# Performance work log

Measured on AMD Instinct MI355X. Metric: run time of the kernel, lower is better.

## Reference

```python
import jax, jax.numpy as jnp
import numpy as np

N = 100000   # num_nodes
E = 1250000  # num_edges
D = 64       # embedding_dim
L = 3        # num_layers


def setup_inputs() -> dict:
    key = jax.random.key(0)
    k1, k2, k3, k4 = jax.random.split(key, 4)
    edge_index = jax.random.randint(k1, (2, E), 0, N, dtype=jnp.int64)
    edge_label_index = jax.random.randint(k2, (2, E), 0, N, dtype=jnp.int64)
    # xavier_uniform init of Embedding(N, D)
    bound = float(np.sqrt(6.0 / (N + D)))
    emb_weight = jax.random.uniform(k3, (N, D), jnp.float32, -bound, bound)
    alpha = jnp.full((L + 1,), 1.0 / (L + 1), dtype=jnp.float32)
    return {"edge_index": edge_index, "edge_label_index": edge_label_index,
            "emb_weight": emb_weight, "alpha": alpha}


def reference(edge_index, edge_label_index, emb_weight, alpha):
    src, dst = edge_index[0], edge_index[1]
    n = emb_weight.shape[0]
    # gcn_norm (LGConv, no self-loops): deg over destination, sym normalization
    deg = jax.ops.segment_sum(jnp.ones(src.shape[0], emb_weight.dtype), dst, num_segments=n)
    dis = jnp.where(deg > 0, jax.lax.rsqrt(jnp.where(deg > 0, deg, 1.0)), 0.0)
    w = dis[src] * dis[dst]  # [E]

    weights = jax.nn.softmax(alpha)  # [L+1]
    x = emb_weight
    out = x * weights[0]
    for i in range(L):
        # LGConv: out[dst] += norm * x[src]
        x = jax.ops.segment_sum(w[:, None] * x[src], dst, num_segments=n)
        out = out + x * weights[i + 1]

    # predict_link_embedding: per-edge dot product
    return (out[edge_label_index[0]] * out[edge_label_index[1]]).sum(axis=-1)
```

## Files before the change

kernel.cpp:

```cpp
#include <hip/hip_runtime.h>
#include <math.h>

#define DIM 64
#define PART_T 2048
#define BK_SHIFT 9
#define BK_SPAN 512
#define BK_CAP 8192
#define BK_PAD 2048
#define BK_REG (BK_CAP + BK_PAD)
#define CSR_T 1024

typedef _Float16 half8 __attribute__((ext_vector_type(8)));


__device__ __forceinline__ half8 shfl_xor_h8(half8 v, int mask) {
    int4 iv;
    __builtin_memcpy(&iv, &v, 16);
    iv.x = __shfl_xor(iv.x, mask, 64);
    iv.y = __shfl_xor(iv.y, mask, 64);
    iv.z = __shfl_xor(iv.z, mask, 64);
    iv.w = __shfl_xor(iv.w, mask, 64);
    half8 r;
    __builtin_memcpy(&r, &iv, 16);
    return r;
}

__device__ __forceinline__ half8 dpp_ror8_h8(half8 v) {
    int4 iv;
    __builtin_memcpy(&iv, &v, 16);
    int4 r;
    r.x = __builtin_amdgcn_update_dpp(0, iv.x, 0x128, 0xF, 0xF, true);
    r.y = __builtin_amdgcn_update_dpp(0, iv.y, 0x128, 0xF, 0xF, true);
    r.z = __builtin_amdgcn_update_dpp(0, iv.z, 0x128, 0xF, 0xF, true);
    r.w = __builtin_amdgcn_update_dpp(0, iv.w, 0x128, 0xF, 0xF, true);
    half8 out;
    __builtin_memcpy(&out, &r, 16);
    return out;
}

__device__ __forceinline__ float dpp_sum8_f32(float v) {
    int x = __float_as_int(v);
    v += __int_as_float(__builtin_amdgcn_update_dpp(0, x, 0xB1, 0xF, 0xF, true));
    x = __float_as_int(v);
    v += __int_as_float(__builtin_amdgcn_update_dpp(0, x, 0x4E, 0xF, 0xF, true));
    x = __float_as_int(v);
    v += __int_as_float(__builtin_amdgcn_update_dpp(0, x, 0x141, 0xF, 0xF, true));
    return v;
}

__device__ __forceinline__ int wave_incl_scan(int v) {
    int lane = threadIdx.x & 63;
    #pragma unroll
    for (int d = 1; d < 64; d <<= 1) {
        int n = __shfl_up(v, d, 64);
        if (lane >= d) v += n;
    }
    return v;
}

__device__ __forceinline__ int block_scan_excl(int v, int* wsum) {
    int incl = wave_incl_scan(v);
    int w = threadIdx.x >> 6;
    if ((threadIdx.x & 63) == 63) wsum[w] = incl;
    __syncthreads();
    int offset = 0;
    #pragma unroll
    for (int i = 0; i < 3; ++i) offset += (i < w) ? wsum[i] : 0;
    return offset + incl - v;
}

template <int NW>
__device__ __forceinline__ int block_scan_excl_n(int v, int* wsum) {
    int incl = wave_incl_scan(v);
    int w = threadIdx.x >> 6;
    if ((threadIdx.x & 63) == 63) wsum[w] = incl;
    __syncthreads();
    int offset = 0;
    #pragma unroll
    for (int i = 0; i < NW - 1; ++i) offset += (i < w) ? wsum[i] : 0;
    return offset + incl - v;
}


__global__ void init_kernel(int* __restrict__ gcursor, int K,
                            half8* __restrict__ g0, half8* __restrict__ g1,
                            half8* __restrict__ g2, int N) {
    int t = threadIdx.x;
    if (t < K) gcursor[t] = t * BK_CAP;
    if (t < 8) {
        half8 z = (half8)(_Float16)0;
        g0[(size_t)N * 8 + t] = z;
        g1[(size_t)N * 8 + t] = z;
        g2[(size_t)N * 8 + t] = z;
    }
}


__global__ void part_kernel(const int* __restrict__ src, const int* __restrict__ dst,
                            int* __restrict__ gcursor, unsigned int* __restrict__ part,
                            int E, int K) {
    __shared__ unsigned int tmp_rec[PART_T];
    __shared__ unsigned char tmp_bkt[PART_T];
    __shared__ int hist[256];
    __shared__ int lstart[256];
    __shared__ int cursor[256];
    __shared__ int gbase[256];
    __shared__ int wsum[4];
    int t = threadIdx.x;
    int tile = blockIdx.x * PART_T;
    int n = E - tile; if (n > PART_T) n = PART_T;

    hist[t] = 0;
    __syncthreads();

    for (int i = t; i < n; i += 256) {
        int s = src[tile + i];
        int d = dst[tile + i];
        int b = d >> BK_SHIFT;
        tmp_rec[i] = (unsigned int)s | ((unsigned int)(d & (BK_SPAN - 1)) << 17);
        tmp_bkt[i] = (unsigned char)b;
        atomicAdd(&hist[b], 1);
    }
    __syncthreads();

    int hv = hist[t];
    int excl = block_scan_excl(hv, wsum);
    lstart[t] = excl;
    cursor[t] = excl;
    if (t < K && hv > 0) gbase[t] = atomicAdd(&gcursor[t], hv);
    __syncthreads();

    for (int i = t; i < n; i += 256) {
        int b = tmp_bkt[i];
        int r = atomicAdd(&cursor[b], 1);
        part[gbase[b] + (r - lstart[b])] = tmp_rec[i];
    }
}


__global__ __launch_bounds__(CSR_T)
void csr_kernel(const unsigned int* __restrict__ part, const int* __restrict__ gcursor,
                int2* __restrict__ prange, int* __restrict__ csr_src,
                float* __restrict__ dis,
                const float* __restrict__ emb, half8* __restrict__ g0, int N) {
    __shared__ int h[BK_SPAN];
    __shared__ int pfx[BK_SPAN + 1];
    __shared__ float sdis[BK_SPAN];
    __shared__ int wsum[CSR_T / 64];
    int b = blockIdx.x;
    int t = threadIdx.x;
    int pbase = b * BK_CAP;
    int cnt   = gcursor[b] - pbase;
    int qbase = b * BK_REG;
    int nodeBase = b << BK_SHIFT;

    if (t < BK_SPAN) h[t] = 0;
    __syncthreads();

    for (int j = t; j < cnt; j += CSR_T) {
        unsigned int rec = part[pbase + j];
        atomicAdd(&h[rec >> 17], 1);
    }
    __syncthreads();

    int d0 = (t < BK_SPAN) ? h[t] : 0;
    if (t < BK_SPAN) {
        float f0 = d0 > 0 ? rsqrtf((float)d0) : 0.0f;
        int i0 = nodeBase + t;
        if (i0 < N) dis[i0] = f0;
        sdis[t] = f0;
    }
    int p0 = (d0 + 3) & ~3;
    int excl = block_scan_excl_n<CSR_T / 64>(p0, wsum);
    if (t < BK_SPAN) {
        pfx[t] = excl;
        h[t]   = excl;
    }
    if (t == BK_SPAN - 1) pfx[BK_SPAN] = excl + p0;
    __syncthreads();

    if (t < BK_SPAN) {
        int idx = nodeBase + t;
        if (idx < N) prange[idx] = make_int2(qbase + pfx[t], qbase + pfx[t + 1]);
    }
    __syncthreads();

    for (int j = t; j < cnt; j += CSR_T) {
        unsigned int rec = part[pbase + j];
        int dl = (int)(rec >> 17);
        int s  = (int)(rec & 0x1FFFFu);
        int p = atomicAdd(&h[dl], 1);
        csr_src[qbase + p] = s;
    }
    __syncthreads();

    if (t < BK_SPAN) {
        int endp = pfx[t + 1];
        for (int p = h[t]; p < endp; ++p) csr_src[qbase + p] = N;
    }

    const float4* e4 = (const float4*)emb;
    int nloc = N - nodeBase;
    if (nloc > BK_SPAN) nloc = BK_SPAN;
    int lim = nloc * 8;
    for (int j = t; j < lim; j += CSR_T) {
        int r = j >> 3;
        int v = nodeBase + r;
        float dv = sdis[r];
        float4 a = e4[(size_t)v * 16 + (size_t)(j & 7) * 2];
        float4 c = e4[(size_t)v * 16 + (size_t)(j & 7) * 2 + 1];
        half8 hh;
        hh[0] = (_Float16)(dv * a.x); hh[1] = (_Float16)(dv * a.y);
        hh[2] = (_Float16)(dv * a.z); hh[3] = (_Float16)(dv * a.w);
        hh[4] = (_Float16)(dv * c.x); hh[5] = (_Float16)(dv * c.y);
        hh[6] = (_Float16)(dv * c.z); hh[7] = (_Float16)(dv * c.w);
        g0[(size_t)v * 8 + (j & 7)] = hh;
    }
}


__device__ __forceinline__ void softmax4(const float* __restrict__ alpha, float* w) {
    float a0 = alpha[0], a1 = alpha[1], a2 = alpha[2], a3 = alpha[3];
    float m = fmaxf(fmaxf(a0, a1), fmaxf(a2, a3));
    float e0 = expf(a0 - m), e1 = expf(a1 - m), e2 = expf(a2 - m), e3 = expf(a3 - m);
    float s = 1.0f / (e0 + e1 + e2 + e3);
    w[0] = e0 * s; w[1] = e1 * s; w[2] = e2 * s; w[3] = e3 * s;
}

__global__ void spmm_kernel(const int2* __restrict__ prange, const int* __restrict__ csr_src,
                            const float* __restrict__ dis,
                            const half8* __restrict__ gin, half8* __restrict__ gout, int N) {
    int lane = threadIdx.x & 63;
    int wave = blockIdx.x * (blockDim.x >> 6) + (threadIdx.x >> 6);
    int v = wave * 2 + (lane >> 5);
    int slot = (lane >> 3) & 3;
    int sub  = lane & 7;
    bool valid = v < N;
    int beg = 0, end = 0;
    if (valid) { int2 pr = prange[v]; beg = pr.x; end = pr.y; }
    const int4* csr4 = (const int4*)csr_src;
    half8 acc0 = (half8)(_Float16)0;
    half8 acc1 = (half8)(_Float16)0;
    for (int j = beg + slot * 4; j < end; j += 16) {
        int4 c = csr4[j >> 2];
        acc0 = acc0 + gin[c.x * 8 + sub];
        acc1 = acc1 + gin[c.y * 8 + sub];
        acc0 = acc0 + gin[c.z * 8 + sub];
        acc1 = acc1 + gin[c.w * 8 + sub];
    }
    half8 acc = acc0 + acc1;
    acc = acc + dpp_ror8_h8(acc);
    acc = acc + shfl_xor_h8(acc, 16);
    if (valid && (lane & 31) < 8) {
        float d = dis[v];
        float d2 = d * d;
        half8 o;
        #pragma unroll
        for (int k = 0; k < 8; ++k) o[k] = (_Float16)(d2 * (float)acc[k]);
        gout[v * 8 + sub] = o;
    }
}

__global__ void spmm_final_kernel(const int2* __restrict__ prange, const int* __restrict__ csr_src,
                                  const float* __restrict__ dis,
                                  const float* __restrict__ emb, const half8* __restrict__ g1,
                                  const half8* __restrict__ g2, half8* __restrict__ out,
                                  const float* __restrict__ alpha, int N) {
    int lane = threadIdx.x & 63;
    int wave = blockIdx.x * (blockDim.x >> 6) + (threadIdx.x >> 6);
    int v = wave * 2 + (lane >> 5);
    int slot = (lane >> 3) & 3;
    int sub  = lane & 7;
    bool valid = v < N;
    int beg = 0, end = 0;
    if (valid) { int2 pr = prange[v]; beg = pr.x; end = pr.y; }
    const int4* csr4 = (const int4*)csr_src;
    half8 acc0 = (half8)(_Float16)0;
    half8 acc1 = (half8)(_Float16)0;
    for (int j = beg + slot * 4; j < end; j += 16) {
        int4 c = csr4[j >> 2];
        acc0 = acc0 + g2[c.x * 8 + sub];
        acc1 = acc1 + g2[c.y * 8 + sub];
        acc0 = acc0 + g2[c.z * 8 + sub];
        acc1 = acc1 + g2[c.w * 8 + sub];
    }
    half8 acc = acc0 + acc1;
    acc = acc + dpp_ror8_h8(acc);
    acc = acc + shfl_xor_h8(acc, 16);
    if (valid && (lane & 31) < 8) {
        float w[4];
        softmax4(alpha, w);
        float d  = dis[v];
        float iv = d > 0.0f ? 1.0f / d : 0.0f;
        const float4* e4 = (const float4*)emb;
        float4 ea = e4[v * 16 + sub * 2];
        float4 eb = e4[v * 16 + sub * 2 + 1];
        half8 h1 = g1[v * 8 + sub];
        half8 h2 = g2[v * 8 + sub];
        float ef[8] = {ea.x, ea.y, ea.z, ea.w, eb.x, eb.y, eb.z, eb.w};
        half8 o;
        #pragma unroll
        for (int k = 0; k < 8; ++k) {
            float x1 = (float)h1[k] * iv;
            float x2 = (float)h2[k] * iv;
            float x3 = d * (float)acc[k];
            float val = w[0] * ef[k] + w[1] * x1 + w[2] * x2 + w[3] * x3;
            o[k] = (_Float16)val;
        }
        out[v * 8 + sub] = o;
    }
}

__global__ void dot_kernel(const int* __restrict__ a, const int* __restrict__ b,
                           const half8* __restrict__ out, float* __restrict__ res, int E) {
    long long g = (long long)blockIdx.x * blockDim.x + threadIdx.x;
    int e   = (int)(g >> 3);
    int sub = (int)(g & 7);
    if (e >= E) return;
    int ia = a[e];
    int ib = b[e];
    half8 va = out[ia * 8 + sub];
    half8 vb = out[ib * 8 + sub];
#if __has_builtin(__builtin_amdgcn_fdot2)
    float v = 0.f;
    v = __builtin_amdgcn_fdot2(__builtin_shufflevector(va, va, 0, 1),
                               __builtin_shufflevector(vb, vb, 0, 1), v, false);
    v = __builtin_amdgcn_fdot2(__builtin_shufflevector(va, va, 2, 3),
                               __builtin_shufflevector(vb, vb, 2, 3), v, false);
    v = __builtin_amdgcn_fdot2(__builtin_shufflevector(va, va, 4, 5),
                               __builtin_shufflevector(vb, vb, 4, 5), v, false);
    v = __builtin_amdgcn_fdot2(__builtin_shufflevector(va, va, 6, 7),
                               __builtin_shufflevector(vb, vb, 6, 7), v, false);
#else
    float v = 0.f;
    #pragma unroll
    for (int k = 0; k < 8; ++k) v += (float)va[k] * (float)vb[k];
#endif
    v = dpp_sum8_f32(v);
    if (sub == 0) res[e] = v;
}


static inline size_t align256(size_t x) { return (x + 255) & ~(size_t)255; }

extern "C" void kernel_launch(void* const* d_in, const int* in_sizes, int n_in,
                              void* d_out, int out_size, void* d_ws, size_t ws_size,
                              hipStream_t stream) {
    const int* edge_index = (const int*)d_in[0];
    const int* edge_label = (const int*)d_in[1];
    const float* emb      = (const float*)d_in[2];
    const float* alpha    = (const float*)d_in[3];

    const int E = in_sizes[0] / 2;
    const int N = in_sizes[2] / DIM;
    const int K = (N + BK_SPAN - 1) >> BK_SHIFT;

    const int* src = edge_index;
    const int* dst = edge_index + E;
    const int* la  = edge_label;
    const int* lb  = edge_label + E;

    char* ws = (char*)d_ws;
    size_t off = 0;
    float* dis     = (float*)(ws + off); off = align256(off + (size_t)N * 4);
    int2*  prange  = (int2*)(ws + off);  off = align256(off + (size_t)N * 8);
    int*   gcursor = (int*)(ws + off);   off = align256(off + (size_t)256 * 4);
    unsigned int* part = (unsigned int*)(ws + off); off = align256(off + (size_t)K * BK_CAP * 4);
    int*   csr_src = (int*)(ws + off);   off = align256(off + (size_t)K * BK_REG * 4);
    half8* g0      = (half8*)(ws + off); off = align256(off + (size_t)(N + 1) * DIM * 2);
    half8* g1      = (half8*)(ws + off); off = align256(off + (size_t)(N + 1) * DIM * 2);
    half8* g2      = (half8*)(ws + off); off = align256(off + (size_t)(N + 1) * DIM * 2);
    half8* outbuf  = g0;
    (void)ws_size;

    const int B = 256;
    const int gridT = (E + PART_T - 1) / PART_T;

    init_kernel<<<1, B, 0, stream>>>(gcursor, K, g0, g1, g2, N);

    part_kernel<<<gridT, B, 0, stream>>>(src, dst, gcursor, part, E, K);

    csr_kernel<<<K, CSR_T, 0, stream>>>(part, gcursor, prange, csr_src, dis, emb, g0, N);

    const int nodesPerBlock = (B / 64) * 2;
    const int gridS = (N + nodesPerBlock - 1) / nodesPerBlock;
    spmm_kernel<<<gridS, B, 0, stream>>>(prange, csr_src, dis, g0, g1, N);
    spmm_kernel<<<gridS, B, 0, stream>>>(prange, csr_src, dis, g1, g2, N);
    spmm_final_kernel<<<gridS, B, 0, stream>>>(prange, csr_src, dis, emb, g1, g2,
                                               outbuf, alpha, N);

    const long long dthreads = (long long)E * 8;
    const int gridD = (int)((dthreads + B - 1) / B);
    dot_kernel<<<gridD, B, 0, stream>>>(la, lb, outbuf, (float*)d_out, E);
}
```

Before: 230.4 us.

## Split feature dimension into four column slices for cache-resident gathers

Re-lays out the fp16 node feature buffers as four 16-column slices, each stored contiguously over all nodes. Each SpMM layer and the final dot product are launched once per slice, so the working set of each gather is a quarter of the full table and more of it can stay in cache. In exchange, the CSR indices and row ranges are read four times, there are four times as many launches, and the dot output is accumulated through read-modify-write passes.

```diff
diff --git a/kernel.cpp b/kernel.cpp
--- a/kernel.cpp
+++ b/kernel.cpp
@@ -11,6 +11,7 @@
 #define CSR_T 1024
 
 typedef _Float16 half8 __attribute__((ext_vector_type(8)));
+
 
 
 __device__ __forceinline__ half8 shfl_xor_h8(half8 v, int mask) {
@@ -25,29 +26,6 @@
     return r;
 }
 
-__device__ __forceinline__ half8 dpp_ror8_h8(half8 v) {
-    int4 iv;
-    __builtin_memcpy(&iv, &v, 16);
-    int4 r;
-    r.x = __builtin_amdgcn_update_dpp(0, iv.x, 0x128, 0xF, 0xF, true);
-    r.y = __builtin_amdgcn_update_dpp(0, iv.y, 0x128, 0xF, 0xF, true);
-    r.z = __builtin_amdgcn_update_dpp(0, iv.z, 0x128, 0xF, 0xF, true);
-    r.w = __builtin_amdgcn_update_dpp(0, iv.w, 0x128, 0xF, 0xF, true);
-    half8 out;
-    __builtin_memcpy(&out, &r, 16);
-    return out;
-}
-
-__device__ __forceinline__ float dpp_sum8_f32(float v) {
-    int x = __float_as_int(v);
-    v += __int_as_float(__builtin_amdgcn_update_dpp(0, x, 0xB1, 0xF, 0xF, true));
-    x = __float_as_int(v);
-    v += __int_as_float(__builtin_amdgcn_update_dpp(0, x, 0x4E, 0xF, 0xF, true));
-    x = __float_as_int(v);
-    v += __int_as_float(__builtin_amdgcn_update_dpp(0, x, 0x141, 0xF, 0xF, true));
-    return v;
-}
-
 __device__ __forceinline__ int wave_incl_scan(int v) {
     int lane = threadIdx.x & 63;
     #pragma unroll
@@ -89,9 +67,10 @@
     if (t < K) gcursor[t] = t * BK_CAP;
     if (t < 8) {
         half8 z = (half8)(_Float16)0;
-        g0[(size_t)N * 8 + t] = z;
-        g1[(size_t)N * 8 + t] = z;
-        g2[(size_t)N * 8 + t] = z;
+        size_t idx = ((size_t)(t >> 1) * (N + 1) + N) * 2 + (t & 1);
+        g0[idx] = z;
+        g1[idx] = z;
+        g2[idx] = z;
     }
 }
 
@@ -202,22 +181,59 @@
     const float4* e4 = (const float4*)emb;
     int nloc = N - nodeBase;
     if (nloc > BK_SPAN) nloc = BK_SPAN;
+    if (nloc < 0) nloc = 0;
     int lim = nloc * 8;
     for (int j = t; j < lim; j += CSR_T) {
-        int r = j >> 3;
+        int r   = j >> 3;
+        int sub = j & 7;
         int v = nodeBase + r;
         float dv = sdis[r];
-        float4 a = e4[(size_t)v * 16 + (size_t)(j & 7) * 2];
-        float4 c = e4[(size_t)v * 16 + (size_t)(j & 7) * 2 + 1];
+        float4 a = e4[(size_t)v * 16 + (size_t)sub * 2];
+        float4 c = e4[(size_t)v * 16 + (size_t)sub * 2 + 1];
         half8 hh;
         hh[0] = (_Float16)(dv * a.x); hh[1] = (_Float16)(dv * a.y);
         hh[2] = (_Float16)(dv * a.z); hh[3] = (_Float16)(dv * a.w);
         hh[4] = (_Float16)(dv * c.x); hh[5] = (_Float16)(dv * c.y);
         hh[6] = (_Float16)(dv * c.z); hh[7] = (_Float16)(dv * c.w);
-        g0[(size_t)v * 8 + (j & 7)] = hh;
-    }
-}
-
+        int q  = sub >> 1;
+        int hp = sub & 1;
+        g0[((size_t)q * (N + 1) + v) * 2 + hp] = hh;
+    }
+}
+
+
+__global__ __launch_bounds__(256)
+void spmm_q_kernel(const int2* __restrict__ prange, const int* __restrict__ csr_src,
+                   const float* __restrict__ dis,
+                   const half8* __restrict__ gin, half8* __restrict__ gout,
+                   int N, int q) {
+    int lane = threadIdx.x & 63;
+    int wave = blockIdx.x * (blockDim.x >> 6) + (threadIdx.x >> 6);
+    int v = wave * 2 + (lane >> 5);
+    int slot = (lane >> 1) & 15;
+    int sub  = lane & 1;
+    bool valid = v < N;
+    int beg = 0, end = 0;
+    if (valid) { int2 pr = prange[v]; beg = pr.x; end = pr.y; }
+    const half8* gq = gin + (size_t)q * (N + 1) * 2;
+    half8 acc = (half8)(_Float16)0;
+    for (int j = beg + slot; j < end; j += 16) {
+        int s = csr_src[j];
+        acc = acc + gq[(size_t)s * 2 + sub];
+    }
+    acc = acc + shfl_xor_h8(acc, 2);
+    acc = acc + shfl_xor_h8(acc, 4);
+    acc = acc + shfl_xor_h8(acc, 8);
+    acc = acc + shfl_xor_h8(acc, 16);
+    if (valid && (lane & 31) < 2) {
+        float d = dis[v];
+        float d2 = d * d;
+        half8 o;
+        #pragma unroll
+        for (int k = 0; k < 8; ++k) o[k] = (_Float16)(d2 * (float)acc[k]);
+        gout[((size_t)q * (N + 1) + v) * 2 + sub] = o;
+    }
+}
 
 __device__ __forceinline__ void softmax4(const float* __restrict__ alpha, float* w) {
     float a0 = alpha[0], a1 = alpha[1], a2 = alpha[2], a3 = alpha[3];
@@ -227,76 +243,41 @@
     w[0] = e0 * s; w[1] = e1 * s; w[2] = e2 * s; w[3] = e3 * s;
 }
 
-__global__ void spmm_kernel(const int2* __restrict__ prange, const int* __restrict__ csr_src,
-                            const float* __restrict__ dis,
-                            const half8* __restrict__ gin, half8* __restrict__ gout, int N) {
+__global__ __launch_bounds__(256)
+void spmm_final_q_kernel(const int2* __restrict__ prange, const int* __restrict__ csr_src,
+                         const float* __restrict__ dis,
+                         const float* __restrict__ emb, const half8* __restrict__ g1,
+                         const half8* __restrict__ g2, half8* __restrict__ out,
+                         const float* __restrict__ alpha, int N, int q) {
     int lane = threadIdx.x & 63;
     int wave = blockIdx.x * (blockDim.x >> 6) + (threadIdx.x >> 6);
     int v = wave * 2 + (lane >> 5);
-    int slot = (lane >> 3) & 3;
-    int sub  = lane & 7;
+    int slot = (lane >> 1) & 15;
+    int sub  = lane & 1;
     bool valid = v < N;
     int beg = 0, end = 0;
     if (valid) { int2 pr = prange[v]; beg = pr.x; end = pr.y; }
-    const int4* csr4 = (const int4*)csr_src;
-    half8 acc0 = (half8)(_Float16)0;
-    half8 acc1 = (half8)(_Float16)0;
-    for (int j = beg + slot * 4; j < end; j += 16) {
-        int4 c = csr4[j >> 2];
-        acc0 = acc0 + gin[c.x * 8 + sub];
-        acc1 = acc1 + gin[c.y * 8 + sub];
-        acc0 = acc0 + gin[c.z * 8 + sub];
-        acc1 = acc1 + gin[c.w * 8 + sub];
-    }
-    half8 acc = acc0 + acc1;
-    acc = acc + dpp_ror8_h8(acc);
+    const half8* g2q = g2 + (size_t)q * (N + 1) * 2;
+    half8 acc = (half8)(_Float16)0;
+    for (int j = beg + slot; j < end; j += 16) {
+        int s = csr_src[j];
+        acc = acc + g2q[(size_t)s * 2 + sub];
+    }
+    acc = acc + shfl_xor_h8(acc, 2);
+    acc = acc + shfl_xor_h8(acc, 4);
+    acc = acc + shfl_xor_h8(acc, 8);
     acc = acc + shfl_xor_h8(acc, 16);
-    if (valid && (lane & 31) < 8) {
-        float d = dis[v];
-        float d2 = d * d;
-        half8 o;
-        #pragma unroll
-        for (int k = 0; k < 8; ++k) o[k] = (_Float16)(d2 * (float)acc[k]);
-        gout[v * 8 + sub] = o;
-    }
-}
-
-__global__ void spmm_final_kernel(const int2* __restrict__ prange, const int* __restrict__ csr_src,
-                                  const float* __restrict__ dis,
-                                  const float* __restrict__ emb, const half8* __restrict__ g1,
-                                  const half8* __restrict__ g2, half8* __restrict__ out,
-                                  const float* __restrict__ alpha, int N) {
-    int lane = threadIdx.x & 63;
-    int wave = blockIdx.x * (blockDim.x >> 6) + (threadIdx.x >> 6);
-    int v = wave * 2 + (lane >> 5);
-    int slot = (lane >> 3) & 3;
-    int sub  = lane & 7;
-    bool valid = v < N;
-    int beg = 0, end = 0;
-    if (valid) { int2 pr = prange[v]; beg = pr.x; end = pr.y; }
-    const int4* csr4 = (const int4*)csr_src;
-    half8 acc0 = (half8)(_Float16)0;
-    half8 acc1 = (half8)(_Float16)0;
-    for (int j = beg + slot * 4; j < end; j += 16) {
-        int4 c = csr4[j >> 2];
-        acc0 = acc0 + g2[c.x * 8 + sub];
-        acc1 = acc1 + g2[c.y * 8 + sub];
-        acc0 = acc0 + g2[c.z * 8 + sub];
-        acc1 = acc1 + g2[c.w * 8 + sub];
-    }
-    half8 acc = acc0 + acc1;
-    acc = acc + dpp_ror8_h8(acc);
-    acc = acc + shfl_xor_h8(acc, 16);
-    if (valid && (lane & 31) < 8) {
+    if (valid && (lane & 31) < 2) {
         float w[4];
         softmax4(alpha, w);
         float d  = dis[v];
         float iv = d > 0.0f ? 1.0f / d : 0.0f;
         const float4* e4 = (const float4*)emb;
-        float4 ea = e4[v * 16 + sub * 2];
-        float4 eb = e4[v * 16 + sub * 2 + 1];
-        half8 h1 = g1[v * 8 + sub];
-        half8 h2 = g2[v * 8 + sub];
+        float4 ea = e4[(size_t)v * 16 + q * 4 + sub * 2];
+        float4 eb = e4[(size_t)v * 16 + q * 4 + sub * 2 + 1];
+        size_t ridx = ((size_t)q * (N + 1) + v) * 2 + sub;
+        half8 h1 = g1[ridx];
+        half8 h2 = g2[ridx];
         float ef[8] = {ea.x, ea.y, ea.z, ea.w, eb.x, eb.y, eb.z, eb.w};
         half8 o;
         #pragma unroll
@@ -307,20 +288,22 @@
             float val = w[0] * ef[k] + w[1] * x1 + w[2] * x2 + w[3] * x3;
             o[k] = (_Float16)val;
         }
-        out[v * 8 + sub] = o;
-    }
-}
-
-__global__ void dot_kernel(const int* __restrict__ a, const int* __restrict__ b,
-                           const half8* __restrict__ out, float* __restrict__ res, int E) {
+        out[ridx] = o;
+    }
+}
+
+__global__ void dot_q_kernel(const int* __restrict__ a, const int* __restrict__ b,
+                             const half8* __restrict__ out, float* __restrict__ res,
+                             int E, int N, int q) {
     long long g = (long long)blockIdx.x * blockDim.x + threadIdx.x;
-    int e   = (int)(g >> 3);
-    int sub = (int)(g & 7);
+    int e   = (int)(g >> 1);
+    int sub = (int)(g & 1);
     if (e >= E) return;
     int ia = a[e];
     int ib = b[e];
-    half8 va = out[ia * 8 + sub];
-    half8 vb = out[ib * 8 + sub];
+    const half8* oq = out + (size_t)q * (N + 1) * 2;
+    half8 va = oq[(size_t)ia * 2 + sub];
+    half8 vb = oq[(size_t)ib * 2 + sub];
 #if __has_builtin(__builtin_amdgcn_fdot2)
     float v = 0.f;
     v = __builtin_amdgcn_fdot2(__builtin_shufflevector(va, va, 0, 1),
@@ -336,8 +319,11 @@
     #pragma unroll
     for (int k = 0; k < 8; ++k) v += (float)va[k] * (float)vb[k];
 #endif
-    v = dpp_sum8_f32(v);
-    if (sub == 0) res[e] = v;
+    v += __shfl_xor(v, 1, 64);
+    if (sub == 0) {
+        if (q == 0) res[e] = v;
+        else        res[e] += v;
+    }
 }
 
 
@@ -384,12 +370,16 @@
 
     const int nodesPerBlock = (B / 64) * 2;
     const int gridS = (N + nodesPerBlock - 1) / nodesPerBlock;
-    spmm_kernel<<<gridS, B, 0, stream>>>(prange, csr_src, dis, g0, g1, N);
-    spmm_kernel<<<gridS, B, 0, stream>>>(prange, csr_src, dis, g1, g2, N);
-    spmm_final_kernel<<<gridS, B, 0, stream>>>(prange, csr_src, dis, emb, g1, g2,
-                                               outbuf, alpha, N);
-
-    const long long dthreads = (long long)E * 8;
+    for (int q = 0; q < 4; ++q)
+        spmm_q_kernel<<<gridS, B, 0, stream>>>(prange, csr_src, dis, g0, g1, N, q);
+    for (int q = 0; q < 4; ++q)
+        spmm_q_kernel<<<gridS, B, 0, stream>>>(prange, csr_src, dis, g1, g2, N, q);
+    for (int q = 0; q < 4; ++q)
+        spmm_final_q_kernel<<<gridS, B, 0, stream>>>(prange, csr_src, dis, emb, g1, g2,
+                                                     outbuf, alpha, N, q);
+
+    const long long dthreads = (long long)E * 2;
     const int gridD = (int)((dthreads + B - 1) / B);
-    dot_kernel<<<gridD, B, 0, stream>>>(la, lb, outbuf, (float*)d_out, E);
-}
+    for (int q = 0; q < 4; ++q)
+        dot_q_kernel<<<gridD, B, 0, stream>>>(la, lb, outbuf, (float*)d_out, E, N, q);
+}
```

New measurement: 416.7 us. +80.8%, slower.

## Fuse SpMM layers and dot product into one cooperative persistent kernel

Applied to the files above, without the earlier changes.

Replaces the three SpMM launches and the dot-product launch with a single cooperative kernel. It runs a fixed grid of 1024 blocks as grid-stride persistent waves and separates the phases with grid.sync(). The aim is to remove kernel launch gaps and tail effects between the dependent stages. In exchange, grid-wide barriers and a fixed grid size may lower occupancy or load balance compared with oversubscribed launches. The old separate-kernel path remains as a fallback if the cooperative launch fails.

```diff
diff --git a/kernel.cpp b/kernel.cpp
--- a/kernel.cpp
+++ b/kernel.cpp
@@ -1,5 +1,8 @@
 #include <hip/hip_runtime.h>
+#include <hip/hip_cooperative_groups.h>
 #include <math.h>
+
+namespace cg = cooperative_groups;
 
 #define DIM 64
 #define PART_T 2048
@@ -9,6 +12,8 @@
 #define BK_PAD 2048
 #define BK_REG (BK_CAP + BK_PAD)
 #define CSR_T 1024
+#define FUSE_GRID 1024
+#define FUSE_T 256
 
 typedef _Float16 half8 __attribute__((ext_vector_type(8)));
 
@@ -202,6 +207,7 @@
     const float4* e4 = (const float4*)emb;
     int nloc = N - nodeBase;
     if (nloc > BK_SPAN) nloc = BK_SPAN;
+    if (nloc < 0) nloc = 0;
     int lim = nloc * 8;
     for (int j = t; j < lim; j += CSR_T) {
         int r = j >> 3;
@@ -227,38 +233,161 @@
     w[0] = e0 * s; w[1] = e1 * s; w[2] = e2 * s; w[3] = e3 * s;
 }
 
+__device__ __forceinline__ void spmm_phase(const int2* __restrict__ prange,
+                                           const int* __restrict__ csr_src,
+                                           const float* __restrict__ dis,
+                                           const half8* __restrict__ gin,
+                                           half8* __restrict__ gout,
+                                           int N, int gw, int nwaves) {
+    int lane = threadIdx.x & 63;
+    int hlf  = lane >> 5;
+    int slot = (lane >> 3) & 3;
+    int sub  = lane & 7;
+    const int4* csr4 = (const int4*)csr_src;
+    int npairs = (N + 1) >> 1;
+    for (int p = gw; p < npairs; p += nwaves) {
+        int v = p * 2 + hlf;
+        int2 pr = (v < N) ? prange[v] : make_int2(0, 0);
+        half8 acc0 = (half8)(_Float16)0;
+        half8 acc1 = (half8)(_Float16)0;
+        for (int j = pr.x + slot * 4; j < pr.y; j += 16) {
+            int4 c = csr4[j >> 2];
+            acc0 = acc0 + gin[c.x * 8 + sub];
+            acc1 = acc1 + gin[c.y * 8 + sub];
+            acc0 = acc0 + gin[c.z * 8 + sub];
+            acc1 = acc1 + gin[c.w * 8 + sub];
+        }
+        half8 acc = acc0 + acc1;
+        acc = acc + dpp_ror8_h8(acc);
+        acc = acc + shfl_xor_h8(acc, 16);
+        if (v < N && (lane & 31) < 8) {
+            float d = dis[v];
+            float d2 = d * d;
+            half8 o;
+            #pragma unroll
+            for (int k = 0; k < 8; ++k) o[k] = (_Float16)(d2 * (float)acc[k]);
+            gout[v * 8 + sub] = o;
+        }
+    }
+}
+
+__device__ __forceinline__ void final_phase(const int2* __restrict__ prange,
+                                            const int* __restrict__ csr_src,
+                                            const float* __restrict__ dis,
+                                            const float* __restrict__ emb,
+                                            const half8* __restrict__ g1,
+                                            const half8* __restrict__ g2,
+                                            half8* __restrict__ out,
+                                            const float* __restrict__ alpha,
+                                            int N, int gw, int nwaves) {
+    int lane = threadIdx.x & 63;
+    int hlf  = lane >> 5;
+    int slot = (lane >> 3) & 3;
+    int sub  = lane & 7;
+    const int4* csr4 = (const int4*)csr_src;
+    const float4* e4 = (const float4*)emb;
+    int npairs = (N + 1) >> 1;
+    float w[4];
+    softmax4(alpha, w);
+    for (int p = gw; p < npairs; p += nwaves) {
+        int v = p * 2 + hlf;
+        int2 pr = (v < N) ? prange[v] : make_int2(0, 0);
+        half8 acc0 = (half8)(_Float16)0;
+        half8 acc1 = (half8)(_Float16)0;
+        for (int j = pr.x + slot * 4; j < pr.y; j += 16) {
+            int4 c = csr4[j >> 2];
+            acc0 = acc0 + g2[c.x * 8 + sub];
+            acc1 = acc1 + g2[c.y * 8 + sub];
+            acc0 = acc0 + g2[c.z * 8 + sub];
+            acc1 = acc1 + g2[c.w * 8 + sub];
+        }
+        half8 acc = acc0 + acc1;
+        acc = acc + dpp_ror8_h8(acc);
+        acc = acc + shfl_xor_h8(acc, 16);
+        if (v < N && (lane & 31) < 8) {
+            float d  = dis[v];
+            float iv = d > 0.0f ? 1.0f / d : 0.0f;
+            float4 ea = e4[(size_t)v * 16 + sub * 2];
+            float4 eb = e4[(size_t)v * 16 + sub * 2 + 1];
+            half8 h1 = g1[v * 8 + sub];
+            half8 h2 = g2[v * 8 + sub];
+            float ef[8] = {ea.x, ea.y, ea.z, ea.w, eb.x, eb.y, eb.z, eb.w};
+            half8 o;
+            #pragma unroll
+            for (int k = 0; k < 8; ++k) {
+                float x1 = (float)h1[k] * iv;
+                float x2 = (float)h2[k] * iv;
+                float x3 = d * (float)acc[k];
+                float val = w[0] * ef[k] + w[1] * x1 + w[2] * x2 + w[3] * x3;
+                o[k] = (_Float16)val;
+            }
+            out[v * 8 + sub] = o;
+        }
+    }
+}
+
+__device__ __forceinline__ void dot_phase(const int* __restrict__ la,
+                                          const int* __restrict__ lb,
+                                          const half8* __restrict__ out,
+                                          float* __restrict__ res,
+                                          int E, long long gi0, long long stride) {
+    long long total = (long long)E * 8;
+    int sub = (int)(gi0 & 7);
+    for (long long g = gi0; g < total; g += stride) {
+        int e = (int)(g >> 3);
+        int ia = la[e];
+        int ib = lb[e];
+        half8 va = out[(size_t)ia * 8 + sub];
+        half8 vb = out[(size_t)ib * 8 + sub];
+#if __has_builtin(__builtin_amdgcn_fdot2)
+        float v = 0.f;
+        v = __builtin_amdgcn_fdot2(__builtin_shufflevector(va, va, 0, 1),
+                                   __builtin_shufflevector(vb, vb, 0, 1), v, false);
+        v = __builtin_amdgcn_fdot2(__builtin_shufflevector(va, va, 2, 3),
+                                   __builtin_shufflevector(vb, vb, 2, 3), v, false);
+        v = __builtin_amdgcn_fdot2(__builtin_shufflevector(va, va, 4, 5),
+                                   __builtin_shufflevector(vb, vb, 4, 5), v, false);
+        v = __builtin_amdgcn_fdot2(__builtin_shufflevector(va, va, 6, 7),
+                                   __builtin_shufflevector(vb, vb, 6, 7), v, false);
+#else
+        float v = 0.f;
+        #pragma unroll
+        for (int k = 0; k < 8; ++k) v += (float)va[k] * (float)vb[k];
+#endif
+        v = dpp_sum8_f32(v);
+        if (sub == 0) res[e] = v;
+    }
+}
+
+
+__global__ __launch_bounds__(FUSE_T, 4)
+void fused_kernel(const int2* __restrict__ prange, const int* __restrict__ csr_src,
+                  const float* __restrict__ dis, const float* __restrict__ emb,
+                  half8* __restrict__ g0, half8* __restrict__ g1, half8* __restrict__ g2,
+                  half8* __restrict__ out, const float* __restrict__ alpha,
+                  const int* __restrict__ la, const int* __restrict__ lb,
+                  float* __restrict__ res, int N, int E) {
+    cg::grid_group grid = cg::this_grid();
+    int gw = blockIdx.x * (FUSE_T >> 6) + (threadIdx.x >> 6);
+    const int nwaves = (int)gridDim.x * (FUSE_T >> 6);
+
+    spmm_phase(prange, csr_src, dis, g0, g1, N, gw, nwaves);
+    grid.sync();
+    spmm_phase(prange, csr_src, dis, g1, g2, N, gw, nwaves);
+    grid.sync();
+    final_phase(prange, csr_src, dis, emb, g1, g2, out, alpha, N, gw, nwaves);
+    grid.sync();
+    long long stride = (long long)gridDim.x * FUSE_T;
+    long long gi0    = (long long)blockIdx.x * FUSE_T + threadIdx.x;
+    dot_phase(la, lb, out, res, E, gi0, stride);
+}
+
+
 __global__ void spmm_kernel(const int2* __restrict__ prange, const int* __restrict__ csr_src,
                             const float* __restrict__ dis,
                             const half8* __restrict__ gin, half8* __restrict__ gout, int N) {
-    int lane = threadIdx.x & 63;
-    int wave = blockIdx.x * (blockDim.x >> 6) + (threadIdx.x >> 6);
-    int v = wave * 2 + (lane >> 5);
-    int slot = (lane >> 3) & 3;
-    int sub  = lane & 7;
-    bool valid = v < N;
-    int beg = 0, end = 0;
-    if (valid) { int2 pr = prange[v]; beg = pr.x; end = pr.y; }
-    const int4* csr4 = (const int4*)csr_src;
-    half8 acc0 = (half8)(_Float16)0;
-    half8 acc1 = (half8)(_Float16)0;
-    for (int j = beg + slot * 4; j < end; j += 16) {
-        int4 c = csr4[j >> 2];
-        acc0 = acc0 + gin[c.x * 8 + sub];
-        acc1 = acc1 + gin[c.y * 8 + sub];
-        acc0 = acc0 + gin[c.z * 8 + sub];
-        acc1 = acc1 + gin[c.w * 8 + sub];
-    }
-    half8 acc = acc0 + acc1;
-    acc = acc + dpp_ror8_h8(acc);
-    acc = acc + shfl_xor_h8(acc, 16);
-    if (valid && (lane & 31) < 8) {
-        float d = dis[v];
-        float d2 = d * d;
-        half8 o;
-        #pragma unroll
-        for (int k = 0; k < 8; ++k) o[k] = (_Float16)(d2 * (float)acc[k]);
-        gout[v * 8 + sub] = o;
-    }
+    int gw = blockIdx.x * (blockDim.x >> 6) + (threadIdx.x >> 6);
+    spmm_phase(prange, csr_src, dis, gin, gout, N, gw, 0x40000000);
 }
 
 __global__ void spmm_final_kernel(const int2* __restrict__ prange, const int* __restrict__ csr_src,
@@ -266,78 +395,16 @@
                                   const float* __restrict__ emb, const half8* __restrict__ g1,
                                   const half8* __restrict__ g2, half8* __restrict__ out,
                                   const float* __restrict__ alpha, int N) {
-    int lane = threadIdx.x & 63;
-    int wave = blockIdx.x * (blockDim.x >> 6) + (threadIdx.x >> 6);
-    int v = wave * 2 + (lane >> 5);
-    int slot = (lane >> 3) & 3;
-    int sub  = lane & 7;
-    bool valid = v < N;
-    int beg = 0, end = 0;
-    if (valid) { int2 pr = prange[v]; beg = pr.x; end = pr.y; }
-    const int4* csr4 = (const int4*)csr_src;
-    half8 acc0 = (half8)(_Float16)0;
-    half8 acc1 = (half8)(_Float16)0;
-    for (int j = beg + slot * 4; j < end; j += 16) {
-        int4 c = csr4[j >> 2];
-        acc0 = acc0 + g2[c.x * 8 + sub];
-        acc1 = acc1 + g2[c.y * 8 + sub];
-        acc0 = acc0 + g2[c.z * 8 + sub];
-        acc1 = acc1 + g2[c.w * 8 + sub];
-    }
-    half8 acc = acc0 + acc1;
-    acc = acc + dpp_ror8_h8(acc);
-    acc = acc + shfl_xor_h8(acc, 16);
-    if (valid && (lane & 31) < 8) {
-        float w[4];
-        softmax4(alpha, w);
-        float d  = dis[v];
-        float iv = d > 0.0f ? 1.0f / d : 0.0f;
-        const float4* e4 = (const float4*)emb;
-        float4 ea = e4[v * 16 + sub * 2];
-        float4 eb = e4[v * 16 + sub * 2 + 1];
-        half8 h1 = g1[v * 8 + sub];
-        half8 h2 = g2[v * 8 + sub];
-        float ef[8] = {ea.x, ea.y, ea.z, ea.w, eb.x, eb.y, eb.z, eb.w};
-        half8 o;
-        #pragma unroll
-        for (int k = 0; k < 8; ++k) {
-            float x1 = (float)h1[k] * iv;
-            float x2 = (float)h2[k] * iv;
-            float x3 = d * (float)acc[k];
-            float val = w[0] * ef[k] + w[1] * x1 + w[2] * x2 + w[3] * x3;
-            o[k] = (_Float16)val;
-        }
-        out[v * 8 + sub] = o;
-    }
+    int gw = blockIdx.x * (blockDim.x >> 6) + (threadIdx.x >> 6);
+    final_phase(prange, csr_src, dis, emb, g1, g2, out, alpha, N, gw, 0x40000000);
 }
 
 __global__ void dot_kernel(const int* __restrict__ a, const int* __restrict__ b,
                            const half8* __restrict__ out, float* __restrict__ res, int E) {
-    long long g = (long long)blockIdx.x * blockDim.x + threadIdx.x;
-    int e   = (int)(g >> 3);
-    int sub = (int)(g & 7);
-    if (e >= E) return;
-    int ia = a[e];
-    int ib = b[e];
-    half8 va = out[ia * 8 + sub];
-    half8 vb = out[ib * 8 + sub];
-#if __has_builtin(__builtin_amdgcn_fdot2)
-    float v = 0.f;
-    v = __builtin_amdgcn_fdot2(__builtin_shufflevector(va, va, 0, 1),
-                               __builtin_shufflevector(vb, vb, 0, 1), v, false);
-    v = __builtin_amdgcn_fdot2(__builtin_shufflevector(va, va, 2, 3),
-                               __builtin_shufflevector(vb, vb, 2, 3), v, false);
-    v = __builtin_amdgcn_fdot2(__builtin_shufflevector(va, va, 4, 5),
-                               __builtin_shufflevector(vb, vb, 4, 5), v, false);
-    v = __builtin_amdgcn_fdot2(__builtin_shufflevector(va, va, 6, 7),
-                               __builtin_shufflevector(vb, vb, 6, 7), v, false);
-#else
-    float v = 0.f;
-    #pragma unroll
-    for (int k = 0; k < 8; ++k) v += (float)va[k] * (float)vb[k];
-#endif
-    v = dpp_sum8_f32(v);
-    if (sub == 0) res[e] = v;
+    long long gi0 = (long long)blockIdx.x * blockDim.x + threadIdx.x;
+    long long total = (long long)E * 8;
+    if (gi0 >= total) return;
+    dot_phase(a, b, out, res, E, gi0, (long long)1 << 62);
 }
 
 
@@ -382,14 +449,28 @@
 
     csr_kernel<<<K, CSR_T, 0, stream>>>(part, gcursor, prange, csr_src, dis, emb, g0, N);
 
-    const int nodesPerBlock = (B / 64) * 2;
-    const int gridS = (N + nodesPerBlock - 1) / nodesPerBlock;
-    spmm_kernel<<<gridS, B, 0, stream>>>(prange, csr_src, dis, g0, g1, N);
-    spmm_kernel<<<gridS, B, 0, stream>>>(prange, csr_src, dis, g1, g2, N);
-    spmm_final_kernel<<<gridS, B, 0, stream>>>(prange, csr_src, dis, emb, g1, g2,
-                                               outbuf, alpha, N);
-
-    const long long dthreads = (long long)E * 8;
-    const int gridD = (int)((dthreads + B - 1) / B);
-    dot_kernel<<<gridD, B, 0, stream>>>(la, lb, outbuf, (float*)d_out, E);
-}
+    {
+        float* res = (float*)d_out;
+        int Nv = N, Ev = E;
+        void* args[] = {
+            (void*)&prange, (void*)&csr_src, (void*)&dis, (void*)&emb,
+            (void*)&g0, (void*)&g1, (void*)&g2, (void*)&outbuf, (void*)&alpha,
+            (void*)&la, (void*)&lb, (void*)&res, (void*)&Nv, (void*)&Ev
+        };
+        hipError_t err = hipLaunchCooperativeKernel((const void*)fused_kernel,
+                                                    dim3(FUSE_GRID), dim3(FUSE_T),
+                                                    args, 0, stream);
+        if (err != hipSuccess) {
+            (void)hipGetLastError();
+            const int nodesPerBlock = (B / 64) * 2;
+            const int gridS = (N + nodesPerBlock - 1) / nodesPerBlock;
+            spmm_kernel<<<gridS, B, 0, stream>>>(prange, csr_src, dis, g0, g1, N);
+            spmm_kernel<<<gridS, B, 0, stream>>>(prange, csr_src, dis, g1, g2, N);
+            spmm_final_kernel<<<gridS, B, 0, stream>>>(prange, csr_src, dis, emb, g1, g2,
+                                                       outbuf, alpha, N);
+            const long long dthreads = (long long)E * 8;
+            const int gridD = (int)((dthreads + B - 1) / B);
+            dot_kernel<<<gridD, B, 0, stream>>>(la, lb, outbuf, (float*)d_out, E);
+        }
+    }
+}
```

New measurement: 604.0 us. 2.62x slower.
